# Kernel optimization log

Hardware: AMD Instinct MI355X
Metric: run time of the kernel (lower is better)

The kernel has to match this reference:

```python
import jax, jax.numpy as jnp
import numpy as np

T, D, F, G, H = 364, 512, 28, 30000, 128
CIN = 2 * D + F + 1  # 1053


def setup_inputs() -> dict:
    key = jax.random.key(0)
    k = jax.random.split(key, 12)
    s = 0.02  # weight scale so activations stay in a sane range
    return {
        "emb_table": jax.random.normal(k[0], (T, D), jnp.float32),
        "Wp": jax.random.normal(k[1], (D, CIN), jnp.float32) * s,
        "bp": jnp.zeros((D,), jnp.float32),
        "W_ih": jax.random.normal(k[2], (3 * D, D), jnp.float32) * s,
        "b_ih": jnp.zeros((3 * D,), jnp.float32),
        "W_hh": jax.random.normal(k[3], (3 * D, D), jnp.float32) * s,
        "b_hh": jnp.zeros((3 * D,), jnp.float32),
        "ln_g": jnp.ones((D,), jnp.float32),
        "ln_b": jnp.zeros((D,), jnp.float32),
        "Wi1": jax.random.normal(k[4], (H, D), jnp.float32) * s,
        "bi1": jnp.zeros((H,), jnp.float32),
        "Wi2": jax.random.normal(k[5], (1, H), jnp.float32) * s,
        "bi2": jnp.zeros((1,), jnp.float32),
        "features_a": jax.random.normal(k[6], (G, F), jnp.float32),
        "features_b": jax.random.normal(k[7], (G, F), jnp.float32),
        "team_a": jax.random.randint(k[8], (G,), 0, T),
        "team_b": jax.random.randint(k[9], (G,), 0, T),
        "a_won": jax.random.randint(k[10], (G,), 0, 2),
    }


def reference(emb_table, Wp, bp, W_ih, b_ih, W_hh, b_hh, ln_g, ln_b,
              Wi1, bi1, Wi2, bi2, features_a, features_b,
              team_a, team_b, a_won):
    def step(emb, x):
        ta, tb, fa, fb, aw = x
        aw = aw.astype(jnp.float32)
        # both directions of the game processed together as a batch of 2
        e_self = jnp.stack([emb[ta], emb[tb]])                 # [2, D]
        e_opp = e_self[::-1]                                   # [2, D]
        won = jnp.stack([aw, 1.0 - aw])[:, None]               # [2, 1]
        comb = jnp.concatenate([e_self, e_opp, jnp.stack([fa, fb]), won], axis=-1)  # [2, CIN]
        proj = jax.nn.relu(comb @ Wp.T + bp)                   # dropout = identity (eval)
        imp = jax.nn.sigmoid(jax.nn.relu(proj @ Wi1.T + bi1) @ Wi2.T + bi2)  # [2, 1]
        # torch GRUCell
        gi = proj @ W_ih.T + b_ih                              # [2, 3D]
        gh = e_self @ W_hh.T + b_hh
        i_r, i_z, i_n = jnp.split(gi, 3, axis=-1)
        h_r, h_z, h_n = jnp.split(gh, 3, axis=-1)
        r = jax.nn.sigmoid(i_r + h_r)
        z = jax.nn.sigmoid(i_z + h_z)
        n = jnp.tanh(i_n + r * h_n)
        new_h = (1.0 - z) * n + z * e_self
        upd = e_self + imp * (new_h - e_self)
        # LayerNorm(eps=1e-5)
        mu = jnp.mean(upd, axis=-1, keepdims=True)
        var = jnp.mean((upd - mu) ** 2, axis=-1, keepdims=True)
        upd = (upd - mu) / jnp.sqrt(var + 1e-5) * ln_g + ln_b
        emb = emb.at[ta].set(upd[0]).at[tb].set(upd[1])
        return emb, jax.lax.stop_gradient(proj)                # game_context is detached

    final_emb, contexts = jax.lax.scan(
        step, emb_table, (team_a, team_b, features_a, features_b, a_won))
    return final_emb, contexts  # [T, D], [G, 2, D]
```

## Files before the change

kernel.cpp:

```cpp
#include <hip/hip_runtime.h>
#include <math.h>


#define NG   30000
#define NT   364
#define ND   512
#define NF   28
#define NH   128
#define NCIN 1053
#define NB   256
#define BLK  1024
#define WCAP 192

__device__ __forceinline__ float sigmf(float x) { return 1.0f / (1.0f + expf(-x)); }

__device__ __forceinline__ void astore_f(float* p, float v) {
  __hip_atomic_store(p, v, __ATOMIC_RELAXED, __HIP_MEMORY_SCOPE_AGENT);
}
__device__ __forceinline__ void astore_f2(float* p, float x, float y) {
  float2 v = make_float2(x, y);
  unsigned long long u; __builtin_memcpy(&u, &v, 8);
  __hip_atomic_store((unsigned long long*)p, u, __ATOMIC_RELAXED, __HIP_MEMORY_SCOPE_AGENT);
}

__global__ void zero_kernel(int* p, int n) {
  int i = blockIdx.x * blockDim.x + threadIdx.x;
  if (i < n) p[i] = 0;
}

__global__ void deps_kernel(const int* __restrict__ ta, const int* __restrict__ tb,
                            int* __restrict__ dep0, int* __restrict__ dep1) {
  int g = blockIdx.x * blockDim.x + threadIdx.x;
  if (g >= NG) return;
  int a = ta[g], b = tb[g];
  int d0 = -1, d1 = -1;
  for (int p = g - 1; p >= 0; --p) {
    int pa = ta[p], pb = tb[p];
    if (d0 < 0 && (pa == a || pb == a)) d0 = p;
    if (d1 < 0 && (pa == b || pb == b)) d1 = p;
    if (d0 >= 0 && d1 >= 0) break;
  }
  dep0[g] = d0;
  dep1[g] = d1;
}

__global__ void levels_kernel(const int* __restrict__ d0a, const int* __restrict__ d1a,
                              int* __restrict__ level, int* __restrict__ nLevels) {
  __shared__ int lv[1024];
  __shared__ int changed;
  __shared__ int smax;
  const int tid = threadIdx.x;
  int localMax = 0;
  if (tid == 0) smax = 0;
  for (int base = 0; base < NG; base += 1024) {
    const int g = base + tid;
    const bool val = g < NG;
    int ic0 = -1, ic1 = -1, b = 0;
    if (val) {
      int d0 = d0a[g], d1 = d1a[g];
      if (d0 >= 0) { if (d0 < base) b = max(b, level[d0] + 1); else ic0 = d0 - base; }
      if (d1 >= 0) { if (d1 < base) b = max(b, level[d1] + 1); else ic1 = d1 - base; }
    }
    lv[tid] = b;
    __syncthreads();
    for (;;) {
      if (tid == 0) changed = 0;
      __syncthreads();
      int nl = lv[tid];
      if (ic0 >= 0) nl = max(nl, lv[ic0] + 1);
      if (ic1 >= 0) nl = max(nl, lv[ic1] + 1);
      if (val && nl != lv[tid]) { lv[tid] = nl; changed = 1; }
      __syncthreads();
      if (!changed) break;
    }
    if (val) { level[g] = lv[tid]; localMax = max(localMax, lv[tid]); }
    __syncthreads();
  }
  atomicMax(&smax, localMax);
  __syncthreads();
  if (tid == 0) nLevels[0] = smax + 1;
}

__global__ void sort_kernel(const int* __restrict__ level, const int* __restrict__ nLevels,
                            int* __restrict__ hist, int* __restrict__ cursor,
                            int* __restrict__ levelStart, int* __restrict__ levelList) {
  const int tid = threadIdx.x;
  const int nL = nLevels[0];
  for (int i = tid; i < NG; i += 1024) { hist[i] = 0; cursor[i] = 0; }
  __syncthreads();
  for (int g = tid; g < NG; g += 1024) atomicAdd(&hist[level[g]], 1);
  __syncthreads();
  if (tid == 0) {
    int acc = 0;
    for (int i = 0; i < nL; ++i) { levelStart[i] = acc; acc += hist[i]; }
    levelStart[nL] = acc;
  }
  __syncthreads();
  for (int g = tid; g < NG; g += 1024) {
    int l = level[g];
    int off = atomicAdd(&cursor[l], 1);
    levelList[levelStart[l] + off] = g;
  }
}

__device__ __forceinline__ void grid_bar(int* go, int* arr, int& epoch) {
  ++epoch;
  __syncthreads();
  if (blockIdx.x == 0) {
    const int t = threadIdx.x;
    if (t >= 1 && t < NB) {
      while (__hip_atomic_load(arr + t * 32, __ATOMIC_RELAXED, __HIP_MEMORY_SCOPE_AGENT) < epoch)
        __builtin_amdgcn_s_sleep(1);
    }
    __builtin_amdgcn_fence(__ATOMIC_ACQUIRE, "agent");
    __syncthreads();
    if (t == 0)
      __hip_atomic_store(go, epoch, __ATOMIC_RELEASE, __HIP_MEMORY_SCOPE_AGENT);
  } else {
    if (threadIdx.x == 0) {
      __hip_atomic_store(arr + blockIdx.x * 32, epoch, __ATOMIC_RELEASE, __HIP_MEMORY_SCOPE_AGENT);
      while (__hip_atomic_load(go, __ATOMIC_RELAXED, __HIP_MEMORY_SCOPE_AGENT) < epoch)
        __builtin_amdgcn_s_sleep(1);
      __builtin_amdgcn_fence(__ATOMIC_ACQUIRE, "agent");
    }
    __syncthreads();
  }
}

__global__ __launch_bounds__(BLK, 4)
void game_kernel(const float* __restrict__ Wp,   const float* __restrict__ bp,
                 const float* __restrict__ W_ih, const float* __restrict__ b_ih,
                 const float* __restrict__ W_hh, const float* __restrict__ b_hh,
                 const float* __restrict__ ln_g, const float* __restrict__ ln_b,
                 const float* __restrict__ Wi1,  const float* __restrict__ bi1,
                 const float* __restrict__ Wi2,  const float* __restrict__ bi2,
                 const float* __restrict__ fA,   const float* __restrict__ fB,
                 const int* __restrict__ team_a, const int* __restrict__ team_b,
                 const int* __restrict__ a_won,
                 float* __restrict__ emb, float* __restrict__ ctx,
                 const int* __restrict__ levelStart, const int* __restrict__ levelList,
                 const int* __restrict__ nLevels,
                 float* __restrict__ nhbuf, float* __restrict__ hidbuf,
                 int* __restrict__ go, int* __restrict__ arr, int Wcap) {
  const int b    = blockIdx.x;
  const int tid  = threadIdx.x;
  const int lane = tid & 63;
  const int wave = tid >> 6;
  const int grpq = lane >> 4;
  const int l4   = lane & 15;
  const int d0   = 2 * b;
  const int r_b  = b >> 7;
  const int h_b  = b & 127;

  __shared__ float4 wpS4[256];
  __shared__ float4 wpO4[256];
  __shared__ float2 wpT2[32];
  __shared__ float4 wih4[768];
  __shared__ float4 whh4[768];
  __shared__ float2 wi12[256];
  __shared__ float4 sStash[WCAP][4];
  __shared__ float sImp[2];
  __shared__ float sRed[2][16];
  __shared__ float sStat[4];

  if (tid < 256) {
    const int p = tid;
    wpS4[p] = make_float4(Wp[(size_t)d0 * NCIN + 2 * p],
                          Wp[(size_t)(d0 + 1) * NCIN + 2 * p],
                          Wp[(size_t)d0 * NCIN + 2 * p + 1],
                          Wp[(size_t)(d0 + 1) * NCIN + 2 * p + 1]);
    wpO4[p] = make_float4(Wp[(size_t)d0 * NCIN + ND + 2 * p],
                          Wp[(size_t)(d0 + 1) * NCIN + ND + 2 * p],
                          Wp[(size_t)d0 * NCIN + ND + 2 * p + 1],
                          Wp[(size_t)(d0 + 1) * NCIN + ND + 2 * p + 1]);
    wi12[p] = make_float2(Wi1[(size_t)h_b * ND + 2 * p],
                          Wi1[(size_t)h_b * ND + 2 * p + 1]);
  } else if (tid < 288) {
    const int t = tid - 256;
    wpT2[t] = (t < NF + 1)
        ? make_float2(Wp[(size_t)d0 * NCIN + 2 * ND + t],
                      Wp[(size_t)(d0 + 1) * NCIN + 2 * ND + t])
        : make_float2(0.f, 0.f);
  }
  if (tid < 768) {
    const int gt = tid >> 8, p = tid & 255;
    wih4[tid] = make_float4(W_ih[((size_t)gt * ND + d0) * ND + 2 * p],
                            W_ih[((size_t)gt * ND + d0 + 1) * ND + 2 * p],
                            W_ih[((size_t)gt * ND + d0) * ND + 2 * p + 1],
                            W_ih[((size_t)gt * ND + d0 + 1) * ND + 2 * p + 1]);
    whh4[tid] = make_float4(W_hh[((size_t)gt * ND + d0) * ND + 2 * p],
                            W_hh[((size_t)gt * ND + d0 + 1) * ND + 2 * p],
                            W_hh[((size_t)gt * ND + d0) * ND + 2 * p + 1],
                            W_hh[((size_t)gt * ND + d0 + 1) * ND + 2 * p + 1]);
  }

  const float bp0 = bp[d0], bp1 = bp[d0 + 1];
  float bih[6], bhh[6];
#pragma unroll
  for (int gt = 0; gt < 3; ++gt)
#pragma unroll
    for (int d = 0; d < 2; ++d) {
      bih[gt * 2 + d] = b_ih[gt * ND + d0 + d];
      bhh[gt * 2 + d] = b_hh[gt * ND + d0 + d];
    }
  const float bi1h = bi1[h_b];
  const float bi2v = bi2[0];
  const float2 w2p = ((const float2*)Wi2)[lane];
  float2 lg2 = make_float2(0.f, 0.f), lb2 = lg2;
  if (tid < 512) {
    lg2 = ((const float2*)ln_g)[tid & 255];
    lb2 = ((const float2*)ln_b)[tid & 255];
  }
  __syncthreads();

  const int nL = nLevels[0];
  int epoch = 0;

  for (int L = 0; L < nL; ++L) {
    const int s = levelStart[L], e_ = levelStart[L + 1];
    for (int cs = s; cs < e_; cs += Wcap) {
      const int W = min(e_ - cs, Wcap);

      for (int w = wave * 4 + grpq; w < W; w += 64) {
        const int g = levelList[cs + w];
        const int ta = team_a[g], tb = team_b[g];
        const float aw = (float)a_won[g];
        const float* rowA = emb + (size_t)ta * ND;
        const float* rowB = emb + (size_t)tb * ND;
        const float2 es0 = *(const float2*)(rowA + d0);
        const float2 es1 = *(const float2*)(rowB + d0);
        float acc[16];
#pragma unroll
        for (int i = 0; i < 16; ++i) acc[i] = 0.f;
#pragma unroll 8
        for (int j = 0; j < 16; ++j) {
          const int p = j * 16 + l4;
          const float2 va = *(const float2*)(rowA + 2 * p);
          const float2 vb = *(const float2*)(rowB + 2 * p);
          const float4 wS = wpS4[p];
          const float4 wO = wpO4[p];
          acc[0] += va.x * wS.x + va.y * wS.z + vb.x * wO.x + vb.y * wO.z;
          acc[1] += va.x * wS.y + va.y * wS.w + vb.x * wO.y + vb.y * wO.w;
          acc[2] += vb.x * wS.x + vb.y * wS.z + va.x * wO.x + va.y * wO.z;
          acc[3] += vb.x * wS.y + vb.y * wS.w + va.x * wO.y + va.y * wO.w;
#pragma unroll
          for (int gt = 0; gt < 3; ++gt) {
            const float4 q = whh4[gt * 256 + p];
            acc[4 + gt * 2 + 0]  += va.x * q.x + va.y * q.z;
            acc[4 + gt * 2 + 1]  += va.x * q.y + va.y * q.w;
            acc[10 + gt * 2 + 0] += vb.x * q.x + vb.y * q.z;
            acc[10 + gt * 2 + 1] += vb.x * q.y + vb.y * q.w;
          }
        }
#pragma unroll
        for (int j = 0; j < 2; ++j) {
          const int t = j * 16 + l4;
          if (t < NF + 1) {
            const float cv0 = (t < NF) ? fA[(size_t)g * NF + t] : aw;
            const float cv1 = (t < NF) ? fB[(size_t)g * NF + t] : 1.0f - aw;
            const float2 wt = wpT2[t];
            acc[0] += cv0 * wt.x; acc[1] += cv0 * wt.y;
            acc[2] += cv1 * wt.x; acc[3] += cv1 * wt.y;
          }
        }
#pragma unroll
        for (int off = 8; off > 0; off >>= 1) {
#pragma unroll
          for (int i = 0; i < 16; ++i) acc[i] += __shfl_xor(acc[i], off);
        }
        if (l4 == 0) {
          astore_f2(ctx + (size_t)g * 1024 + d0,
                    fmaxf(acc[0] + bp0, 0.f), fmaxf(acc[1] + bp1, 0.f));
          astore_f2(ctx + (size_t)g * 1024 + ND + d0,
                    fmaxf(acc[2] + bp0, 0.f), fmaxf(acc[3] + bp1, 0.f));
          sStash[w][0] = make_float4(acc[4], acc[5], acc[6], acc[7]);
          sStash[w][1] = make_float4(acc[8], acc[9], es0.x, es0.y);
          sStash[w][2] = make_float4(acc[10], acc[11], acc[12], acc[13]);
          sStash[w][3] = make_float4(acc[14], acc[15], es1.x, es1.y);
        }
      }
      grid_bar(go, arr, epoch);

      for (int w = wave * 4 + grpq; w < W; w += 64) {
        const int g = levelList[cs + w];
        const float* p0 = ctx + (size_t)g * 1024;
        const float* p1 = p0 + ND;
        float acc[13];
#pragma unroll
        for (int i = 0; i < 13; ++i) acc[i] = 0.f;
#pragma unroll 8
        for (int j = 0; j < 16; ++j) {
          const int p = j * 16 + l4;
          const float2 x0 = *(const float2*)(p0 + 2 * p);
          const float2 x1 = *(const float2*)(p1 + 2 * p);
#pragma unroll
          for (int gt = 0; gt < 3; ++gt) {
            const float4 q = wih4[gt * 256 + p];
            acc[gt * 2 + 0]     += x0.x * q.x + x0.y * q.z;
            acc[gt * 2 + 1]     += x0.x * q.y + x0.y * q.w;
            acc[6 + gt * 2 + 0] += x1.x * q.x + x1.y * q.z;
            acc[6 + gt * 2 + 1] += x1.x * q.y + x1.y * q.w;
          }
          const float2 wi = wi12[p];
          const float2 xr = r_b ? x1 : x0;
          acc[12] += xr.x * wi.x + xr.y * wi.y;
        }
#pragma unroll
        for (int off = 8; off > 0; off >>= 1) {
#pragma unroll
          for (int i = 0; i < 13; ++i) acc[i] += __shfl_xor(acc[i], off);
        }
        if (l4 == 0) {
          const float4 s0 = sStash[w][0], s1 = sStash[w][1];
          const float4 s2 = sStash[w][2], s3 = sStash[w][3];
          {
            const float r0 = sigmf(acc[0] + bih[0] + s0.x + bhh[0]);
            const float r1 = sigmf(acc[1] + bih[1] + s0.y + bhh[1]);
            const float z0 = sigmf(acc[2] + bih[2] + s0.z + bhh[2]);
            const float z1 = sigmf(acc[3] + bih[3] + s0.w + bhh[3]);
            const float n0 = tanhf(acc[4] + bih[4] + r0 * (s1.x + bhh[4]));
            const float n1 = tanhf(acc[5] + bih[5] + r1 * (s1.y + bhh[5]));
            astore_f2(nhbuf + (size_t)w * 1024 + d0,
                      (1.f - z0) * n0 + z0 * s1.z,
                      (1.f - z1) * n1 + z1 * s1.w);
          }
          {
            const float r0 = sigmf(acc[6] + bih[0] + s2.x + bhh[0]);
            const float r1 = sigmf(acc[7] + bih[1] + s2.y + bhh[1]);
            const float z0 = sigmf(acc[8] + bih[2] + s2.z + bhh[2]);
            const float z1 = sigmf(acc[9] + bih[3] + s2.w + bhh[3]);
            const float n0 = tanhf(acc[10] + bih[4] + r0 * (s3.x + bhh[4]));
            const float n1 = tanhf(acc[11] + bih[5] + r1 * (s3.y + bhh[5]));
            astore_f2(nhbuf + (size_t)w * 1024 + ND + d0,
                      (1.f - z0) * n0 + z0 * s3.z,
                      (1.f - z1) * n1 + z1 * s3.w);
          }
          astore_f(hidbuf + (size_t)w * 256 + r_b * NH + h_b,
                   fmaxf(acc[12] + bi1h, 0.f));
        }
      }
      grid_bar(go, arr, epoch);

      for (int w = b; w < W; w += NB) {
        const int g = levelList[cs + w];
        const int ta = team_a[g], tb = team_b[g];
        if (wave < 2) {
          const float2 hv = *(const float2*)(hidbuf + (size_t)w * 256 + wave * NH + 2 * lane);
          float a = hv.x * w2p.x + hv.y * w2p.y;
#pragma unroll
          for (int off = 32; off > 0; off >>= 1) a += __shfl_xor(a, off);
          if (lane == 0) sImp[wave] = sigmf(a + bi2v);
        }
        __syncthreads();
        float ux = 0.f, uy = 0.f;
        if (tid < 512) {
          const int row = tid >> 8;
          const int e = 2 * (tid & 255);
          const int team = row ? tb : ta;
          const float imp = sImp[row];
          const float2 ev = *(const float2*)(emb + (size_t)team * ND + e);
          const float2 nv = *(const float2*)(nhbuf + (size_t)w * 1024 + (size_t)row * ND + e);
          ux = ev.x + imp * (nv.x - ev.x);
          uy = ev.y + imp * (nv.y - ev.y);
        }
        float sS = ux + uy, sQ = ux * ux + uy * uy;
#pragma unroll
        for (int off = 32; off > 0; off >>= 1) {
          sS += __shfl_xor(sS, off);
          sQ += __shfl_xor(sQ, off);
        }
        if (lane == 0) { sRed[0][wave] = sS; sRed[1][wave] = sQ; }
        __syncthreads();
        if (tid == 0) {
          const float S0 = sRed[0][0] + sRed[0][1] + sRed[0][2] + sRed[0][3];
          const float Q0 = sRed[1][0] + sRed[1][1] + sRed[1][2] + sRed[1][3];
          const float S1 = sRed[0][4] + sRed[0][5] + sRed[0][6] + sRed[0][7];
          const float Q1 = sRed[1][4] + sRed[1][5] + sRed[1][6] + sRed[1][7];
          const float mu0 = S0 * (1.0f / ND), mu1 = S1 * (1.0f / ND);
          const float v0 = Q0 * (1.0f / ND) - mu0 * mu0;
          const float v1 = Q1 * (1.0f / ND) - mu1 * mu1;
          sStat[0] = mu0; sStat[1] = 1.0f / sqrtf(v0 + 1e-5f);
          sStat[2] = mu1; sStat[3] = 1.0f / sqrtf(v1 + 1e-5f);
        }
        __syncthreads();
        if (tid < 512) {
          const int row = tid >> 8;
          const int e = 2 * (tid & 255);
          const float mu = sStat[row * 2], rs = sStat[row * 2 + 1];
          const float ox = (ux - mu) * rs * lg2.x + lb2.x;
          const float oy = (uy - mu) * rs * lg2.y + lb2.y;
          if (row == 0) {
            if (ta != tb) astore_f2(emb + (size_t)ta * ND + e, ox, oy);
          } else {
            astore_f2(emb + (size_t)tb * ND + e, ox, oy);
          }
        }
        __syncthreads();
      }
      grid_bar(go, arr, epoch);
    }
  }
}

extern "C" void kernel_launch(void* const* d_in, const int* in_sizes, int n_in,
                              void* d_out, int out_size, void* d_ws, size_t ws_size,
                              hipStream_t stream) {
  const float* emb_table = (const float*)d_in[0];
  const float* Wp    = (const float*)d_in[1];
  const float* bp    = (const float*)d_in[2];
  const float* W_ih  = (const float*)d_in[3];
  const float* b_ih  = (const float*)d_in[4];
  const float* W_hh  = (const float*)d_in[5];
  const float* b_hh  = (const float*)d_in[6];
  const float* ln_g  = (const float*)d_in[7];
  const float* ln_b  = (const float*)d_in[8];
  const float* Wi1   = (const float*)d_in[9];
  const float* bi1   = (const float*)d_in[10];
  const float* Wi2   = (const float*)d_in[11];
  const float* bi2   = (const float*)d_in[12];
  const float* fA    = (const float*)d_in[13];
  const float* fB    = (const float*)d_in[14];
  const int*   team_a = (const int*)d_in[15];
  const int*   team_b = (const int*)d_in[16];
  const int*   a_won  = (const int*)d_in[17];

  float* out = (float*)d_out;
  float* emb = out;
  float* ctx = out + (size_t)NT * ND;

  int* ip         = (int*)d_ws;
  int* go         = ip;
  int* arr        = ip + 32;
  int* nLevels    = ip + 32 + NB * 32;
  int* dep0       = nLevels + 32;
  int* dep1       = dep0 + NG;
  int* level      = dep1 + NG;
  int* hist       = level + NG;
  int* cursor     = hist + NG;
  int* levelStart = cursor + NG;
  int* levelList  = levelStart + NG + 2;
  const int flagInts = 32 + NB * 32;
  size_t control = (size_t)((char*)(levelList + NG) - (char*)d_ws);
  control = (control + 255) & ~(size_t)255;

  int Wcap = WCAP;
  {
    size_t avail = (ws_size > control + 4096)
        ? (ws_size - control) / ((size_t)(1024 + 256) * sizeof(float))
        : 8;
    if (avail < (size_t)Wcap) Wcap = (int)avail;
    if (Wcap < 8) Wcap = 8;
  }
  float* nhbuf  = (float*)((char*)d_ws + control);
  float* hidbuf = nhbuf + (size_t)Wcap * 1024;

  hipMemcpyAsync(emb, emb_table, (size_t)NT * ND * sizeof(float),
                 hipMemcpyDeviceToDevice, stream);
  zero_kernel<<<(flagInts + 255) / 256, 256, 0, stream>>>(ip, flagInts);
  deps_kernel<<<(NG + 255) / 256, 256, 0, stream>>>(team_a, team_b, dep0, dep1);
  levels_kernel<<<1, 1024, 0, stream>>>(dep0, dep1, level, nLevels);
  sort_kernel<<<1, 1024, 0, stream>>>(level, nLevels, hist, cursor, levelStart, levelList);
  game_kernel<<<NB, BLK, 0, stream>>>(
      Wp, bp, W_ih, b_ih, W_hh, b_hh, ln_g, ln_b, Wi1, bi1, Wi2, bi2,
      fA, fB, team_a, team_b, a_won, emb, ctx,
      levelStart, levelList, nLevels, nhbuf, hidbuf, go, arr, Wcap);
}
```

Baseline: 23.30 ms.

## Double the persistent grid, split games across block halves, cache game indices in LDS

The persistent grid goes from 256 to 512 blocks. Each output-column pair is now owned by two blocks that split the games of a level chunk between them by parity. Each block also stages the chunk's game ids, team ids and win flags into shared memory once, instead of re-reading them through levelList in every phase. The aim is more parallelism per level and fewer dependent global loads, at the cost of twice as many blocks in each grid barrier and a higher occupancy demand (launch bounds of 8 blocks per CU).

```diff
diff --git a/kernel.cpp b/kernel.cpp
--- a/kernel.cpp
+++ b/kernel.cpp
@@ -8,7 +8,7 @@
 #define NF   28
 #define NH   128
 #define NCIN 1053
-#define NB   256
+#define NB   512
 #define BLK  1024
 #define WCAP 192
 
@@ -127,7 +127,7 @@
   }
 }
 
-__global__ __launch_bounds__(BLK, 4)
+__global__ __launch_bounds__(BLK, 8)
 void game_kernel(const float* __restrict__ Wp,   const float* __restrict__ bp,
                  const float* __restrict__ W_ih, const float* __restrict__ b_ih,
                  const float* __restrict__ W_hh, const float* __restrict__ b_hh,
@@ -148,9 +148,11 @@
   const int wave = tid >> 6;
   const int grpq = lane >> 4;
   const int l4   = lane & 15;
-  const int d0   = 2 * b;
-  const int r_b  = b >> 7;
-  const int h_b  = b & 127;
+  const int pairid = b & 255;
+  const int ghalf  = b >> 8;
+  const int d0   = 2 * pairid;
+  const int r_b  = pairid >> 7;
+  const int h_b  = pairid & 127;
 
   __shared__ float4 wpS4[256];
   __shared__ float4 wpO4[256];
@@ -158,7 +160,9 @@
   __shared__ float4 wih4[768];
   __shared__ float4 whh4[768];
   __shared__ float2 wi12[256];
-  __shared__ float4 sStash[WCAP][4];
+  __shared__ float4 sStash[WCAP / 2][4];
+  __shared__ int   sG[WCAP], sTa[WCAP], sTb[WCAP];
+  __shared__ float sAw[WCAP];
   __shared__ float sImp[2];
   __shared__ float sRed[2][16];
   __shared__ float sStat[4];
@@ -221,10 +225,20 @@
     for (int cs = s; cs < e_; cs += Wcap) {
       const int W = min(e_ - cs, Wcap);
 
-      for (int w = wave * 4 + grpq; w < W; w += 64) {
-        const int g = levelList[cs + w];
-        const int ta = team_a[g], tb = team_b[g];
-        const float aw = (float)a_won[g];
+      if (tid < W) {
+        const int g = levelList[cs + tid];
+        sG[tid] = g;
+        sTa[tid] = team_a[g];
+        sTb[tid] = team_b[g];
+        sAw[tid] = (float)a_won[g];
+      }
+      __syncthreads();
+
+      for (int w = (wave * 4 + grpq) * 2 + ghalf; w < W; w += 128) {
+        const int g = sG[w];
+        const int ta = sTa[w], tb = sTb[w];
+        const float aw = sAw[w];
+        const int sw = w >> 1;
         const float* rowA = emb + (size_t)ta * ND;
         const float* rowB = emb + (size_t)tb * ND;
         const float2 es0 = *(const float2*)(rowA + d0);
@@ -273,16 +287,17 @@
                     fmaxf(acc[0] + bp0, 0.f), fmaxf(acc[1] + bp1, 0.f));
           astore_f2(ctx + (size_t)g * 1024 + ND + d0,
                     fmaxf(acc[2] + bp0, 0.f), fmaxf(acc[3] + bp1, 0.f));
-          sStash[w][0] = make_float4(acc[4], acc[5], acc[6], acc[7]);
-          sStash[w][1] = make_float4(acc[8], acc[9], es0.x, es0.y);
-          sStash[w][2] = make_float4(acc[10], acc[11], acc[12], acc[13]);
-          sStash[w][3] = make_float4(acc[14], acc[15], es1.x, es1.y);
+          sStash[sw][0] = make_float4(acc[4], acc[5], acc[6], acc[7]);
+          sStash[sw][1] = make_float4(acc[8], acc[9], es0.x, es0.y);
+          sStash[sw][2] = make_float4(acc[10], acc[11], acc[12], acc[13]);
+          sStash[sw][3] = make_float4(acc[14], acc[15], es1.x, es1.y);
         }
       }
       grid_bar(go, arr, epoch);
 
-      for (int w = wave * 4 + grpq; w < W; w += 64) {
-        const int g = levelList[cs + w];
+      for (int w = (wave * 4 + grpq) * 2 + ghalf; w < W; w += 128) {
+        const int g = sG[w];
+        const int sw = w >> 1;
         const float* p0 = ctx + (size_t)g * 1024;
         const float* p1 = p0 + ND;
         float acc[13];
@@ -311,8 +326,8 @@
           for (int i = 0; i < 13; ++i) acc[i] += __shfl_xor(acc[i], off);
         }
         if (l4 == 0) {
-          const float4 s0 = sStash[w][0], s1 = sStash[w][1];
-          const float4 s2 = sStash[w][2], s3 = sStash[w][3];
+          const float4 s0 = sStash[sw][0], s1 = sStash[sw][1];
+          const float4 s2 = sStash[sw][2], s3 = sStash[sw][3];
           {
             const float r0 = sigmf(acc[0] + bih[0] + s0.x + bhh[0]);
             const float r1 = sigmf(acc[1] + bih[1] + s0.y + bhh[1]);
@@ -342,8 +357,7 @@
       grid_bar(go, arr, epoch);
 
       for (int w = b; w < W; w += NB) {
-        const int g = levelList[cs + w];
-        const int ta = team_a[g], tb = team_b[g];
+        const int ta = sTa[w], tb = sTb[w];
         if (wave < 2) {
           const float2 hv = *(const float2*)(hidbuf + (size_t)w * 256 + wave * NH + 2 * lane);
           float a = hv.x * w2p.x + hv.y * w2p.y;
```

Result: slower. 46.59 ms (+100.0%).
